# Kernel optimization log

Measured on AMD Instinct MI355X. Metric: run time of the kernel, lower is better.

Reference implementation:

```python
import jax, jax.numpy as jnp
import numpy as np


def _forward(hidden_states, edge_src, edge_tgt, edge_label, gcn_W, gcn_b,
             attn_w, attn_b, ms_W1, ms_b1, ms_w2, ms_b2, ant_w, ant_b, span_width):
    B, S, H = hidden_states.shape
    L = gcn_W.shape[0]
    # ---- GCNLayer: per-label linear on gathered source nodes, scatter-add to targets
    src = edge_src.reshape(-1)
    tgt = edge_tgt.reshape(-1)
    lab = edge_label.reshape(-1)
    E = edge_src.shape[1]
    bidx = jnp.repeat(jnp.arange(B), E)                      # [Et]
    src_emb = hidden_states[bidx, src]                       # [Et, H]
    transformed = jnp.zeros_like(src_emb)
    for l in range(L):                                       # fixed small label set
        y = src_emb @ gcn_W[l].T + gcn_b[l]
        transformed = jnp.where((lab == l)[:, None], y, transformed)
    valid = (lab != -100) & (src < S) & (tgt < S)
    transformed = jnp.where(valid[:, None], transformed, 0.0)
    flat = bidx * S + tgt
    gcn_out = jnp.zeros((B * S, H), hidden_states.dtype).at[flat].add(transformed)
    gcn_out = jax.nn.relu(gcn_out.reshape(B, S, H))
    embeddings = hidden_states + gcn_out                     # combine_strategy='add'
    # ---- candidate spans: all (i, j), j in [i, min(i+W, S)), static per S
    Wsp = int(span_width)
    i = np.arange(S)[:, None]
    w = np.arange(Wsp)[None, :]
    ok = (i + w) < S
    starts = np.broadcast_to(i, (S, Wsp))[ok]                # [Nsp]
    ends = (i + w)[ok]                                       # [Nsp]
    tok_idx_np = starts[:, None] + np.arange(Wsp)[None, :]   # [Nsp, Wsp]
    tok_mask = jnp.asarray(tok_idx_np <= ends[:, None])
    tok_idx = jnp.asarray(np.minimum(tok_idx_np, S - 1))
    # ---- SpanRepresentation: [start_emb ; end_emb ; attention-pooled]
    span_tok = embeddings[:, tok_idx]                        # [B, Nsp, Wsp, H]
    scores = jnp.einsum('bnwh,h->bnw', span_tok, attn_w) + attn_b[0]
    scores = jnp.where(tok_mask[None], scores, -1e30)
    attn = jax.nn.softmax(scores, axis=-1)                   # softmax over span tokens
    pooled = jnp.einsum('bnw,bnwh->bnh', attn, span_tok)
    span_reps = jnp.concatenate(
        [embeddings[:, jnp.asarray(starts)], embeddings[:, jnp.asarray(ends)], pooled],
        axis=-1)                                             # [B, Nsp, 3H]
    # ---- MentionScorer: Linear -> ReLU -> Linear(.,1)
    hdn = jax.nn.relu(jnp.einsum('bnd,ed->bne', span_reps, ms_W1) + ms_b1)
    mention = jnp.einsum('bne,e->bn', hdn, ms_w2) + ms_b2[0]  # [B, Nsp]
    # ---- prune: k = int(0.4 * seq_len); attention_mask is all ones -> static
    k = int(0.4 * S)
    _, top_idx = jax.lax.top_k(mention, k)
    pruned = jnp.take_along_axis(span_reps, top_idx[..., None], axis=1)  # [B, k, 3H]
    # ---- antecedent scorer: Linear on cat([reps_j, reps_i]) decomposes into two dots
    D = span_reps.shape[-1]
    s_j = pruned @ ant_w[:D]                                 # weight on first (column) slot
    s_i = pruned @ ant_w[D:]                                 # weight on second (row) slot
    ant = s_j[:, None, :] + s_i[:, :, None] + ant_b[0]       # [B, k, k]; ant[b,i,j]
    ant = jnp.concatenate([jnp.zeros((B, k, 1), ant.dtype), ant], axis=-1)
    tri = jnp.triu(jnp.ones((k, k), bool), 0)                # mask j >= i
    mext = jnp.concatenate([jnp.zeros((k, 1), bool), tri], axis=1)
    masked = jnp.where(mext[None], jnp.asarray(-1e10, ant.dtype), ant)
    return jnp.log(jax.nn.softmax(masked, axis=-1) + 1e-10)  # [B, k, k+1]


def setup_inputs() -> dict:
    key = jax.random.key(0)
    ks = jax.random.split(key, 10)
    B, S, H, L, E, W = 2, 256, 768, 50, 512, 10
    return {
        'hidden_states': jax.random.normal(ks[0], (B, S, H), jnp.float32),
        'attention_mask': jnp.ones((B, S), jnp.int32),
        'edge_src': jax.random.randint(ks[1], (B, E), 0, S),
        'edge_tgt': jax.random.randint(ks[2], (B, E), 0, S),
        'edge_label': jax.random.randint(ks[3], (B, E), 0, L),
        'gcn_W': jax.random.normal(ks[4], (L, H, H), jnp.float32) * 0.02,
        'gcn_b': jnp.zeros((L, H), jnp.float32),
        'attn_w': jax.random.normal(ks[5], (H,), jnp.float32) * 0.02,
        'attn_b': jnp.zeros((1,), jnp.float32),
        'ms_W1': jax.random.normal(ks[6], (3 * H, 3 * H), jnp.float32) * 0.02,
        'ms_b1': jnp.zeros((3 * H,), jnp.float32),
        'ms_w2': jax.random.normal(ks[7], (3 * H,), jnp.float32) * 0.02,
        'ms_b2': jnp.zeros((1,), jnp.float32),
        'ant_w': jax.random.normal(ks[8], (6 * H,), jnp.float32) * 0.02,
        'ant_b': jnp.zeros((1,), jnp.float32),
        'span_width': 10,
    }


def reference(hidden_states, attention_mask, edge_src, edge_tgt, edge_label,
              gcn_W, gcn_b, attn_w, attn_b, ms_W1, ms_b1, ms_w2, ms_b2,
              ant_w, ant_b, span_width):
    del attention_mask  # all ones; seq_len == S, so k = int(0.4 * S) is static
    return _forward(hidden_states, edge_src, edge_tgt, edge_label, gcn_W, gcn_b,
                    attn_w, attn_b, ms_W1, ms_b1, ms_w2, ms_b2, ant_w, ant_b, span_width)
```

## Files before the change

kernel.cpp:

```cpp
#include <hip/hip_runtime.h>
#include <math.h>

#define B 2
#define S 256
#define H 768
#define L 50
#define E 512
#define W 10
#define NSPAN 2515
#define KTOP 102
#define D3 2304
#define N6 6912

#define OFF_GOUT ((size_t)0)
#define OFF_EMB  ((size_t)393216)
#define OFF_G    ((size_t)786432)
#define OFF_TOKD ((size_t)4325376)
#define OFF_MENT ((size_t)4329472)
#define OFF_SJ   ((size_t)4334592)
#define OFF_SI   ((size_t)4339712)
#define OFF_INT  ((size_t)4345344)
#define OFF_EMBT ((size_t)4347392)
#define OFF_W1T  ((size_t)4740608)

__global__ __launch_bounds__(1024) void k_group(
    const int* __restrict__ esrc, const int* __restrict__ etgt,
    const int* __restrict__ elab, int* __restrict__ cnt,
    int* __restrict__ off, int* __restrict__ edges) {
    __shared__ int lcnt[L];
    __shared__ int loff[L];
    int t = threadIdx.x;
    if (t < L) lcnt[t] = 0;
    __syncthreads();
    int lab = elab[t], src = esrc[t], tgt = etgt[t];
    bool valid = (lab >= 0) && (lab < L) && (src >= 0) && (src < S) && (tgt >= 0) && (tgt < S);
    int mypos = -1;
    if (valid) mypos = atomicAdd(&lcnt[lab], 1);
    __syncthreads();
    if (t == 0) {
        int acc = 0;
        for (int l = 0; l < L; l++) { loff[l] = acc; acc += lcnt[l]; }
    }
    __syncthreads();
    if (valid) edges[loff[lab] + mypos] = t;
    if (t < L) { cnt[t] = lcnt[t]; off[t] = loff[t]; }
}

__global__ __launch_bounds__(256) void k_trans(
    const float* __restrict__ in, float* __restrict__ out, int R, int C) {
    __shared__ float T[32][33];
    int c0 = blockIdx.x * 32, r0 = blockIdx.y * 32;
    int tid = threadIdx.x;
    int cc = tid & 31, r8 = tid >> 5;
#pragma unroll
    for (int i = 0; i < 4; i++) {
        int rr = r8 + 8 * i;
        T[rr][cc] = in[(size_t)(r0 + rr) * C + c0 + cc];
    }
    __syncthreads();
    int rr2 = tid & 31, c8 = tid >> 5;
#pragma unroll
    for (int i = 0; i < 4; i++) {
        int cc2 = c8 + 8 * i;
        out[(size_t)(c0 + cc2) * R + r0 + rr2] = T[rr2][cc2];
    }
}

#define GK 384
__global__ __launch_bounds__(256) void k_gcn(
    const float* __restrict__ hidden, const float* __restrict__ gcnW,
    const float* __restrict__ gcnb, const int* __restrict__ cnt,
    const int* __restrict__ off, const int* __restrict__ edges,
    const int* __restrict__ esrc, const int* __restrict__ etgt,
    float* __restrict__ gout) {
    int l = blockIdx.y;
    int n = cnt[l];
    if (n == 0) return;
    int row0 = blockIdx.x * 64;
    int kbase = blockIdx.z * GK;
    __shared__ float Ws[32][68];
    __shared__ float Xs[32][34];
    __shared__ int srow[32];
    __shared__ int trow[32];
    int tid = threadIdx.x;
    int tx = tid & 15, ty = tid >> 4;
    int o = off[l];
    for (int e0 = 0; e0 < n; e0 += 32) {
        int nv = min(32, n - e0);
        if (tid < 32) {
            int sr = 0, tr = 0;
            if (tid < nv) {
                int g = edges[o + e0 + tid];
                int bb = g / E;
                sr = (bb * S + esrc[g]) * H;
                tr = (bb * S + etgt[g]) * H;
            }
            srow[tid] = sr;
            trow[tid] = tr;
        }
        __syncthreads();
        float acc[4][2];
#pragma unroll
        for (int r = 0; r < 4; r++) { acc[r][0] = 0.f; acc[r][1] = 0.f; }
        for (int kc = 0; kc < GK; kc += 32) {
            int k0 = kbase + kc;
#pragma unroll
            for (int j = 0; j < 2; j++) {
                int f = tid + 256 * j;
                int r = f >> 3, kq = (f & 7) * 4;
                float4 v = *(const float4*)(gcnW + ((size_t)l * H + row0 + r) * H + k0 + kq);
                Ws[kq + 0][r] = v.x; Ws[kq + 1][r] = v.y;
                Ws[kq + 2][r] = v.z; Ws[kq + 3][r] = v.w;
            }
#pragma unroll
            for (int j = 0; j < 4; j++) {
                int f = tid + 256 * j;
                int e = f >> 5, kk = f & 31;
                Xs[kk][e] = hidden[srow[e] + k0 + kk];
            }
            __syncthreads();
#pragma unroll
            for (int k = 0; k < 32; k++) {
                float4 a = *(const float4*)&Ws[k][ty * 4];
                float2 x2 = *(const float2*)&Xs[k][tx * 2];
                acc[0][0] = fmaf(a.x, x2.x, acc[0][0]);
                acc[1][0] = fmaf(a.y, x2.x, acc[1][0]);
                acc[2][0] = fmaf(a.z, x2.x, acc[2][0]);
                acc[3][0] = fmaf(a.w, x2.x, acc[3][0]);
                acc[0][1] = fmaf(a.x, x2.y, acc[0][1]);
                acc[1][1] = fmaf(a.y, x2.y, acc[1][1]);
                acc[2][1] = fmaf(a.z, x2.y, acc[2][1]);
                acc[3][1] = fmaf(a.w, x2.y, acc[3][1]);
            }
            __syncthreads();
        }
        const float* bp = gcnb + l * H + row0 + ty * 4;
        bool addb = (blockIdx.z == 0);
#pragma unroll
        for (int e = 0; e < 2; e++) {
            int ei = tx * 2 + e;
            if (ei < nv) {
                int base = trow[ei] + row0 + ty * 4;
#pragma unroll
                for (int r = 0; r < 4; r++) {
                    float v = acc[r][e];
                    if (addb) v += bp[r];
                    atomicAdd(&gout[base + r], v);
                }
            }
        }
        __syncthreads();
    }
}

__global__ __launch_bounds__(256) void k_embdots(
    const float* __restrict__ hidden, const float* __restrict__ gout,
    const float* __restrict__ attnw, const float* __restrict__ antw,
    float* __restrict__ emb, float* __restrict__ tokd) {
    int wave = threadIdx.x >> 6, lane = threadIdx.x & 63;
    int tok = blockIdx.x * 4 + wave;
    const float* hp = hidden + (size_t)tok * H;
    const float* gp = gout + (size_t)tok * H;
    float* ep = emb + (size_t)tok * H;
    float p[7] = {0, 0, 0, 0, 0, 0, 0};
#pragma unroll
    for (int m = 0; m < 12; m++) {
        int k = lane + 64 * m;
        float e = hp[k] + fmaxf(gp[k], 0.f);
        ep[k] = e;
        p[0] = fmaf(attnw[k], e, p[0]);
#pragma unroll
        for (int q = 0; q < 6; q++) p[1 + q] = fmaf(antw[q * H + k], e, p[1 + q]);
    }
#pragma unroll
    for (int q = 0; q < 7; q++) {
        float v = p[q];
#pragma unroll
        for (int d = 32; d; d >>= 1) v += __shfl_down(v, d);
        p[q] = v;
    }
    if (lane == 0) {
        float* o = tokd + (size_t)tok * 8;
#pragma unroll
        for (int q = 0; q < 7; q++) o[q] = p[q];
    }
}

__global__ __launch_bounds__(256, 4) void k_gemm(
    const float* __restrict__ embT, const float* __restrict__ W1T, float* __restrict__ G) {
    __shared__ float As[32][68];
    __shared__ float Bs[32][68];
    int n0 = blockIdx.x * 64;
    int m0 = blockIdx.y * 64;
    int blk = n0 / D3;
    int e0 = n0 - blk * D3;
    int tid = threadIdx.x;
    int tx = tid & 15, ty = tid >> 4;
    const float* Ap = embT + m0;
    const float* Bp = W1T + (size_t)(blk * H) * D3 + e0;
    int r0 = tid >> 4, q0 = (tid & 15) * 4;
    int r1 = (tid + 256) >> 4, q1 = ((tid + 256) & 15) * 4;
    float4 pa0 = *(const float4*)(Ap + (size_t)r0 * 512 + q0);
    float4 pa1 = *(const float4*)(Ap + (size_t)r1 * 512 + q1);
    float4 pb0 = *(const float4*)(Bp + (size_t)r0 * D3 + q0);
    float4 pb1 = *(const float4*)(Bp + (size_t)r1 * D3 + q1);
    float c00 = 0.f, c01 = 0.f, c02 = 0.f, c03 = 0.f;
    float c10 = 0.f, c11 = 0.f, c12 = 0.f, c13 = 0.f;
    float c20 = 0.f, c21 = 0.f, c22 = 0.f, c23 = 0.f;
    float c30 = 0.f, c31 = 0.f, c32 = 0.f, c33 = 0.f;
    for (int kt = 0; kt < H; kt += 32) {
        *(float4*)&As[r0][q0] = pa0;
        *(float4*)&As[r1][q1] = pa1;
        *(float4*)&Bs[r0][q0] = pb0;
        *(float4*)&Bs[r1][q1] = pb1;
        __syncthreads();
        if (kt + 32 < H) {
            const float* Apn = Ap + (size_t)(kt + 32) * 512;
            const float* Bpn = Bp + (size_t)(kt + 32) * D3;
            pa0 = *(const float4*)(Apn + (size_t)r0 * 512 + q0);
            pa1 = *(const float4*)(Apn + (size_t)r1 * 512 + q1);
            pb0 = *(const float4*)(Bpn + (size_t)r0 * D3 + q0);
            pb1 = *(const float4*)(Bpn + (size_t)r1 * D3 + q1);
        }
#pragma unroll
        for (int k = 0; k < 32; k++) {
            float4 av = *(const float4*)&As[k][ty * 4];
            float4 bv = *(const float4*)&Bs[k][tx * 4];
            c00 = fmaf(av.x, bv.x, c00); c01 = fmaf(av.x, bv.y, c01);
            c02 = fmaf(av.x, bv.z, c02); c03 = fmaf(av.x, bv.w, c03);
            c10 = fmaf(av.y, bv.x, c10); c11 = fmaf(av.y, bv.y, c11);
            c12 = fmaf(av.y, bv.z, c12); c13 = fmaf(av.y, bv.w, c13);
            c20 = fmaf(av.z, bv.x, c20); c21 = fmaf(av.z, bv.y, c21);
            c22 = fmaf(av.z, bv.z, c22); c23 = fmaf(av.z, bv.w, c23);
            c30 = fmaf(av.w, bv.x, c30); c31 = fmaf(av.w, bv.y, c31);
            c32 = fmaf(av.w, bv.z, c32); c33 = fmaf(av.w, bv.w, c33);
        }
        __syncthreads();
    }
    float* g0 = G + (size_t)(m0 + ty * 4 + 0) * N6 + n0 + tx * 4;
    float* g1 = G + (size_t)(m0 + ty * 4 + 1) * N6 + n0 + tx * 4;
    float* g2 = G + (size_t)(m0 + ty * 4 + 2) * N6 + n0 + tx * 4;
    float* g3 = G + (size_t)(m0 + ty * 4 + 3) * N6 + n0 + tx * 4;
    *(float4*)g0 = make_float4(c00, c01, c02, c03);
    *(float4*)g1 = make_float4(c10, c11, c12, c13);
    *(float4*)g2 = make_float4(c20, c21, c22, c23);
    *(float4*)g3 = make_float4(c30, c31, c32, c33);
}

__global__ __launch_bounds__(256) void k_span(
    const float* __restrict__ G, const float* __restrict__ tokd,
    const float* __restrict__ b1, const float* __restrict__ w2,
    float* __restrict__ ment, float* __restrict__ sjA, float* __restrict__ siA) {
    int ec = blockIdx.x;
    int start = blockIdx.y;
    int b = blockIdx.z;
    int nw = min(W, S - start);
    int tail = S - start;
    int base = (start <= S - W) ? start * W
             : (S - W + 1) * W + ((W - 1) * W / 2 - tail * (tail + 1) / 2);
    __shared__ float aw[W][W + 1];
    int tid = threadIdx.x;
    const float* td = tokd + (size_t)(b * S) * 8;
    if (tid < nw) {
        int w = tid;
        float sc[W];
        float mx = -3.0e38f;
        for (int j = 0; j <= w; j++) { sc[j] = td[(start + j) * 8]; mx = fmaxf(mx, sc[j]); }
        float sum = 0.f;
        for (int j = 0; j <= w; j++) { float e = expf(sc[j] - mx); aw[w][j] = e; sum += e; }
        float inv = 1.f / sum;
        for (int j = 0; j <= w; j++) aw[w][j] *= inv;
        if (ec == 0) {
            float sj = td[start * 8 + 1] + td[(start + w) * 8 + 2];
            float si = td[start * 8 + 4] + td[(start + w) * 8 + 5];
            for (int j = 0; j <= w; j++) {
                sj = fmaf(aw[w][j], td[(start + j) * 8 + 3], sj);
                si = fmaf(aw[w][j], td[(start + j) * 8 + 6], si);
            }
            sjA[b * NSPAN + base + w] = sj;
            siA[b * NSPAN + base + w] = si;
        }
    }
    __syncthreads();
    int e = ec * 256 + tid;
    const float* Gb = G + (size_t)(b * S) * N6;
    float a = Gb[(size_t)start * N6 + e] + b1[e];
    float w2e = w2[e];
    float cj[W], bm[W];
#pragma unroll
    for (int j = 0; j < W; j++) {
        if (j < nw) {
            cj[j] = Gb[(size_t)(start + j) * N6 + 2 * D3 + e];
            bm[j] = Gb[(size_t)(start + j) * N6 + D3 + e];
        } else { cj[j] = 0.f; bm[j] = 0.f; }
    }
    int lane = tid & 63;
#pragma unroll
    for (int w = 0; w < W; w++) {
        float v = 0.f;
        if (w < nw) {
            float pre = a + bm[w];
#pragma unroll
            for (int j = 0; j <= w; j++) pre = fmaf(aw[w][j], cj[j], pre);
            v = fmaxf(pre, 0.f) * w2e;
        }
#pragma unroll
        for (int d = 32; d; d >>= 1) v += __shfl_down(v, d);
        if (lane == 0 && w < nw) atomicAdd(&ment[b * NSPAN + base + w], v);
    }
}

__global__ __launch_bounds__(256) void k_topkant(
    const float* __restrict__ ment, const float* __restrict__ sjA,
    const float* __restrict__ siA, const float* __restrict__ antb,
    float* __restrict__ out) {
    __shared__ unsigned int uv[NSPAN];
    __shared__ int hist[4][256];
    __shared__ int suf[256];
    __shared__ int cand_i[160];
    __shared__ unsigned int cand_u[160];
    __shared__ int ncand;
    __shared__ unsigned int s_prefix;
    __shared__ int s_kk;
    __shared__ float selj[KTOP];
    __shared__ float seli[KTOP];
    int b = blockIdx.x, tid = threadIdx.x;
    int wave = tid >> 6, lane = tid & 63;
    for (int n = tid; n < NSPAN; n += 256) {
        unsigned int u = __float_as_uint(ment[b * NSPAN + n]);
        uv[n] = (u & 0x80000000u) ? ~u : (u | 0x80000000u);
    }
    if (tid == 0) { s_prefix = 0u; s_kk = KTOP; ncand = 0; }
    __syncthreads();
    for (int pass = 3; pass >= 0; pass--) {
        int shift = pass * 8;
#pragma unroll
        for (int q = 0; q < 4; q++) hist[q][tid] = 0;
        __syncthreads();
        unsigned int pref = s_prefix;
        unsigned int pmask = (pass == 3) ? 0u : (0xFFFFFFFFu << (shift + 8));
        for (int n = tid; n < NSPAN; n += 256) {
            unsigned int u = uv[n];
            if ((u & pmask) == pref) atomicAdd(&hist[wave][(u >> shift) & 255], 1);
        }
        __syncthreads();
        suf[tid] = hist[0][tid] + hist[1][tid] + hist[2][tid] + hist[3][tid];
        __syncthreads();
        for (int d2 = 1; d2 < 256; d2 <<= 1) {
            int y = suf[tid] + ((tid + d2 < 256) ? suf[tid + d2] : 0);
            __syncthreads();
            suf[tid] = y;
            __syncthreads();
        }
        int kk = s_kk;
        __syncthreads();
        if (suf[tid] >= kk && (tid == 255 || suf[tid + 1] < kk)) {
            s_prefix = pref | ((unsigned int)tid << shift);
            s_kk = kk - ((tid == 255) ? 0 : suf[tid + 1]);
        }
        __syncthreads();
    }
    unsigned int uk = s_prefix;
    for (int n = tid; n < NSPAN; n += 256) {
        if (uv[n] >= uk) {
            int p = atomicAdd(&ncand, 1);
            if (p < 160) { cand_i[p] = n; cand_u[p] = uv[n]; }
        }
    }
    __syncthreads();
    int nc = min(ncand, 160);
    for (int c = tid; c < nc; c += 256) {
        unsigned int u = cand_u[c];
        int idx = cand_i[c];
        int rank = 0;
        for (int d = 0; d < nc; d++) {
            unsigned int ud = cand_u[d];
            if (ud > u || (ud == u && cand_i[d] < idx)) rank++;
        }
        if (rank < KTOP) {
            selj[rank] = sjA[b * NSPAN + idx];
            seli[rank] = siA[b * NSPAN + idx];
        }
    }
    __syncthreads();
    float ab = antb[0];
    for (int i = wave; i < KTOP; i += 4) {
        float si = seli[i];
        float v0, v1;
        if (lane == 0) v0 = 0.f;
        else {
            int j = lane - 1;
            v0 = (j >= i) ? -1e10f : (selj[j] + si + ab);
        }
        int c1 = lane + 64;
        bool v1ok = (c1 <= KTOP);
        if (v1ok) {
            int j = c1 - 1;
            v1 = (j >= i) ? -1e10f : (selj[j] + si + ab);
        } else v1 = -3.0e38f;
        float mx = fmaxf(v0, v1);
#pragma unroll
        for (int d = 32; d; d >>= 1) mx = fmaxf(mx, __shfl_down(mx, d));
        mx = __shfl(mx, 0);
        float e0 = expf(v0 - mx);
        float e1 = v1ok ? expf(v1 - mx) : 0.f;
        float sm = e0 + e1;
#pragma unroll
        for (int d = 32; d; d >>= 1) sm += __shfl_down(sm, d);
        sm = __shfl(sm, 0);
        float* op = out + (size_t)(b * KTOP + i) * (KTOP + 1);
        op[lane] = logf(e0 / sm + 1e-10f);
        if (v1ok) op[c1] = logf(e1 / sm + 1e-10f);
    }
}

extern "C" void kernel_launch(void* const* d_in, const int* in_sizes, int n_in,
                              void* d_out, int out_size, void* d_ws, size_t ws_size,
                              hipStream_t stream) {
    (void)in_sizes; (void)n_in; (void)out_size; (void)ws_size;
    const float* hidden = (const float*)d_in[0];
    const int*   esrc   = (const int*)d_in[2];
    const int*   etgt   = (const int*)d_in[3];
    const int*   elab   = (const int*)d_in[4];
    const float* gcnW   = (const float*)d_in[5];
    const float* gcnb   = (const float*)d_in[6];
    const float* attnw  = (const float*)d_in[7];
    const float* msW1   = (const float*)d_in[9];
    const float* msb1   = (const float*)d_in[10];
    const float* msw2   = (const float*)d_in[11];
    const float* antw   = (const float*)d_in[13];
    const float* antb   = (const float*)d_in[14];
    float* out = (float*)d_out;

    float* wsf  = (float*)d_ws;
    float* gout = wsf + OFF_GOUT;
    float* emb  = wsf + OFF_EMB;
    float* G    = wsf + OFF_G;
    float* tokd = wsf + OFF_TOKD;
    float* ment = wsf + OFF_MENT;
    float* sjA  = wsf + OFF_SJ;
    float* siA  = wsf + OFF_SI;
    float* embT = wsf + OFF_EMBT;
    float* W1T  = wsf + OFF_W1T;
    int* wsi   = (int*)(wsf + OFF_INT);
    int* cnt   = wsi;
    int* off   = wsi + 64;
    int* edges = wsi + 128;

    hipMemsetAsync(gout, 0, (size_t)B * S * H * sizeof(float), stream);
    hipMemsetAsync(ment, 0, (size_t)B * NSPAN * sizeof(float), stream);
    k_group<<<1, B * E, 0, stream>>>(esrc, etgt, elab, cnt, off, edges);
    k_trans<<<dim3(D3 / 32, D3 / 32), 256, 0, stream>>>(msW1, W1T, D3, D3);
    k_gcn<<<dim3(12, L, 2), 256, 0, stream>>>(hidden, gcnW, gcnb, cnt, off, edges, esrc, etgt, gout);
    k_embdots<<<B * S / 4, 256, 0, stream>>>(hidden, gout, attnw, antw, emb, tokd);
    k_trans<<<dim3(H / 32, (B * S) / 32), 256, 0, stream>>>(emb, embT, B * S, H);
    k_gemm<<<dim3(N6 / 64, (B * S) / 64), 256, 0, stream>>>(embT, W1T, G);
    k_span<<<dim3(D3 / 256, S, B), 256, 0, stream>>>(G, tokd, msb1, msw2, ment, sjA, siA);
    k_topkant<<<B, 256, 0, stream>>>(ment, sjA, siA, antb, out);
}
```

Baseline: 432.9 us.

## Stage span rows in shared memory, vectorize GCN gathers, split GEMM launches

k_span now processes 8 span starts per block and stages the overlapping bm/cj rows of G in shared memory, so each G row is loaded once per block instead of up to 10 times. The GCN kernel gathers hidden rows with float4 loads instead of scalar ones. The two memsets are replaced by a single init kernel, and the GEMM is split into three launches over column blocks. The changes cut redundant global loads, at the cost of about 37KB of shared memory per k_span block (lower occupancy), a serial loop over starts, and extra launch overhead.

```diff
diff --git a/kernel.cpp b/kernel.cpp
--- a/kernel.cpp
+++ b/kernel.cpp
@@ -7,6 +7,7 @@
 #define L 50
 #define E 512
 #define W 10
+#define SG 8
 #define NSPAN 2515
 #define KTOP 102
 #define D3 2304
@@ -22,6 +23,12 @@
 #define OFF_INT  ((size_t)4345344)
 #define OFF_EMBT ((size_t)4347392)
 #define OFF_W1T  ((size_t)4740608)
+
+__global__ __launch_bounds__(256) void k_init(float* __restrict__ gout, float* __restrict__ ment) {
+    int i = blockIdx.x * 256 + threadIdx.x;
+    if (i < B * S * H) gout[i] = 0.f;
+    if (i < B * NSPAN) ment[i] = 0.f;
+}
 
 __global__ __launch_bounds__(1024) void k_group(
     const int* __restrict__ esrc, const int* __restrict__ etgt,
@@ -84,6 +91,7 @@
     __shared__ int trow[32];
     int tid = threadIdx.x;
     int tx = tid & 15, ty = tid >> 4;
+    int ex = tid >> 3, k4 = (tid & 7) * 4;
     int o = off[l];
     for (int e0 = 0; e0 < n; e0 += 32) {
         int nv = min(32, n - e0);
@@ -112,11 +120,10 @@
                 Ws[kq + 0][r] = v.x; Ws[kq + 1][r] = v.y;
                 Ws[kq + 2][r] = v.z; Ws[kq + 3][r] = v.w;
             }
-#pragma unroll
-            for (int j = 0; j < 4; j++) {
-                int f = tid + 256 * j;
-                int e = f >> 5, kk = f & 31;
-                Xs[kk][e] = hidden[srow[e] + k0 + kk];
+            {
+                float4 xv = *(const float4*)(hidden + srow[ex] + k0 + k4);
+                Xs[k4 + 0][ex] = xv.x; Xs[k4 + 1][ex] = xv.y;
+                Xs[k4 + 2][ex] = xv.z; Xs[k4 + 3][ex] = xv.w;
             }
             __syncthreads();
 #pragma unroll
@@ -187,10 +194,11 @@
 }
 
 __global__ __launch_bounds__(256, 4) void k_gemm(
-    const float* __restrict__ embT, const float* __restrict__ W1T, float* __restrict__ G) {
+    const float* __restrict__ embT, const float* __restrict__ W1T,
+    float* __restrict__ G, int n_base) {
     __shared__ float As[32][68];
     __shared__ float Bs[32][68];
-    int n0 = blockIdx.x * 64;
+    int n0 = n_base + blockIdx.x * 64;
     int m0 = blockIdx.y * 64;
     int blk = n0 / D3;
     int e0 = n0 - blk * D3;
@@ -252,61 +260,77 @@
     const float* __restrict__ b1, const float* __restrict__ w2,
     float* __restrict__ ment, float* __restrict__ sjA, float* __restrict__ siA) {
     int ec = blockIdx.x;
-    int start = blockIdx.y;
+    int s0 = blockIdx.y * SG;
     int b = blockIdx.z;
-    int nw = min(W, S - start);
-    int tail = S - start;
-    int base = (start <= S - W) ? start * W
-             : (S - W + 1) * W + ((W - 1) * W / 2 - tail * (tail + 1) / 2);
-    __shared__ float aw[W][W + 1];
     int tid = threadIdx.x;
+    __shared__ float aw[SG][W][W + 1];
+    __shared__ float bmS[SG + W - 1][257];
+    __shared__ float cjS[SG + W - 1][257];
     const float* td = tokd + (size_t)(b * S) * 8;
-    if (tid < nw) {
-        int w = tid;
-        float sc[W];
-        float mx = -3.0e38f;
-        for (int j = 0; j <= w; j++) { sc[j] = td[(start + j) * 8]; mx = fmaxf(mx, sc[j]); }
-        float sum = 0.f;
-        for (int j = 0; j <= w; j++) { float e = expf(sc[j] - mx); aw[w][j] = e; sum += e; }
-        float inv = 1.f / sum;
-        for (int j = 0; j <= w; j++) aw[w][j] *= inv;
-        if (ec == 0) {
-            float sj = td[start * 8 + 1] + td[(start + w) * 8 + 2];
-            float si = td[start * 8 + 4] + td[(start + w) * 8 + 5];
-            for (int j = 0; j <= w; j++) {
-                sj = fmaf(aw[w][j], td[(start + j) * 8 + 3], sj);
-                si = fmaf(aw[w][j], td[(start + j) * 8 + 6], si);
-            }
-            sjA[b * NSPAN + base + w] = sj;
-            siA[b * NSPAN + base + w] = si;
-        }
-    }
-    __syncthreads();
+    const float* Gb = G + (size_t)(b * S) * N6;
     int e = ec * 256 + tid;
-    const float* Gb = G + (size_t)(b * S) * N6;
-    float a = Gb[(size_t)start * N6 + e] + b1[e];
+#pragma unroll
+    for (int r = 0; r < SG + W - 1; r++) {
+        int row = s0 + r; if (row > S - 1) row = S - 1;
+        bmS[r][tid] = Gb[(size_t)row * N6 + D3 + e];
+        cjS[r][tid] = Gb[(size_t)row * N6 + 2 * D3 + e];
+    }
+    if (tid < SG * W) {
+        int sg = tid / W, w = tid % W;
+        int start = s0 + sg;
+        int nw = min(W, S - start);
+        if (w < nw) {
+            float sc[W];
+            float mx = -3.0e38f;
+            for (int j = 0; j <= w; j++) { sc[j] = td[(start + j) * 8]; mx = fmaxf(mx, sc[j]); }
+            float sum = 0.f;
+            for (int j = 0; j <= w; j++) { float ev = expf(sc[j] - mx); aw[sg][w][j] = ev; sum += ev; }
+            float inv = 1.f / sum;
+            for (int j = 0; j <= w; j++) aw[sg][w][j] *= inv;
+            if (ec == 0) {
+                int tail = S - start;
+                int base = (start <= S - W) ? start * W
+                         : (S - W + 1) * W + ((W - 1) * W / 2 - tail * (tail + 1) / 2);
+                float sj = td[start * 8 + 1] + td[(start + w) * 8 + 2];
+                float si = td[start * 8 + 4] + td[(start + w) * 8 + 5];
+                for (int j = 0; j <= w; j++) {
+                    sj = fmaf(aw[sg][w][j], td[(start + j) * 8 + 3], sj);
+                    si = fmaf(aw[sg][w][j], td[(start + j) * 8 + 6], si);
+                }
+                sjA[b * NSPAN + base + w] = sj;
+                siA[b * NSPAN + base + w] = si;
+            }
+        }
+    }
+    __syncthreads();
     float w2e = w2[e];
-    float cj[W], bm[W];
-#pragma unroll
-    for (int j = 0; j < W; j++) {
-        if (j < nw) {
-            cj[j] = Gb[(size_t)(start + j) * N6 + 2 * D3 + e];
-            bm[j] = Gb[(size_t)(start + j) * N6 + D3 + e];
-        } else { cj[j] = 0.f; bm[j] = 0.f; }
-    }
     int lane = tid & 63;
-#pragma unroll
-    for (int w = 0; w < W; w++) {
-        float v = 0.f;
-        if (w < nw) {
-            float pre = a + bm[w];
-#pragma unroll
-            for (int j = 0; j <= w; j++) pre = fmaf(aw[w][j], cj[j], pre);
-            v = fmaxf(pre, 0.f) * w2e;
-        }
-#pragma unroll
-        for (int d = 32; d; d >>= 1) v += __shfl_down(v, d);
-        if (lane == 0 && w < nw) atomicAdd(&ment[b * NSPAN + base + w], v);
+    for (int sg = 0; sg < SG; sg++) {
+        int start = s0 + sg;
+        int nw = min(W, S - start);
+        int tail = S - start;
+        int base = (start <= S - W) ? start * W
+                 : (S - W + 1) * W + ((W - 1) * W / 2 - tail * (tail + 1) / 2);
+        float a = Gb[(size_t)start * N6 + e] + b1[e];
+        float cj[W], bm[W];
+#pragma unroll
+        for (int j = 0; j < W; j++) {
+            if (j < nw) { cj[j] = cjS[sg + j][tid]; bm[j] = bmS[sg + j][tid]; }
+            else { cj[j] = 0.f; bm[j] = 0.f; }
+        }
+#pragma unroll
+        for (int w = 0; w < W; w++) {
+            float v = 0.f;
+            if (w < nw) {
+                float pre = a + bm[w];
+#pragma unroll
+                for (int j = 0; j <= w; j++) pre = fmaf(aw[sg][w][j], cj[j], pre);
+                v = fmaxf(pre, 0.f) * w2e;
+            }
+#pragma unroll
+            for (int d = 32; d; d >>= 1) v += __shfl_down(v, d);
+            if (lane == 0 && w < nw) atomicAdd(&ment[b * NSPAN + base + w], v);
+        }
     }
 }
 
@@ -447,14 +471,15 @@
     int* off   = wsi + 64;
     int* edges = wsi + 128;
 
-    hipMemsetAsync(gout, 0, (size_t)B * S * H * sizeof(float), stream);
-    hipMemsetAsync(ment, 0, (size_t)B * NSPAN * sizeof(float), stream);
+    k_init<<<(B * S * H + 255) / 256, 256, 0, stream>>>(gout, ment);
     k_group<<<1, B * E, 0, stream>>>(esrc, etgt, elab, cnt, off, edges);
     k_trans<<<dim3(D3 / 32, D3 / 32), 256, 0, stream>>>(msW1, W1T, D3, D3);
     k_gcn<<<dim3(12, L, 2), 256, 0, stream>>>(hidden, gcnW, gcnb, cnt, off, edges, esrc, etgt, gout);
     k_embdots<<<B * S / 4, 256, 0, stream>>>(hidden, gout, attnw, antw, emb, tokd);
     k_trans<<<dim3(H / 32, (B * S) / 32), 256, 0, stream>>>(emb, embT, B * S, H);
-    k_gemm<<<dim3(N6 / 64, (B * S) / 64), 256, 0, stream>>>(embT, W1T, G);
-    k_span<<<dim3(D3 / 256, S, B), 256, 0, stream>>>(G, tokd, msb1, msw2, ment, sjA, siA);
+    k_gemm<<<dim3(D3 / 64, (B * S) / 64), 256, 0, stream>>>(embT, W1T, G, 0);
+    k_gemm<<<dim3(D3 / 64, (B * S) / 64), 256, 0, stream>>>(embT, W1T, G, D3);
+    k_gemm<<<dim3(D3 / 64, (B * S) / 64), 256, 0, stream>>>(embT, W1T, G, 2 * D3);
+    k_span<<<dim3(D3 / 256, S / SG, B), 256, 0, stream>>>(G, tokd, msb1, msw2, ment, sjA, siA);
     k_topkant<<<B, 256, 0, stream>>>(ment, sjA, siA, antb, out);
 }
```

Measured after the change: 485.8 us. 1.12x slower.
